# Optimization experiments

Hardware: AMD Instinct MI355X
Metric: run time of the kernel (lower is better)

The kernel has to match this reference:

```python
import jax, jax.numpy as jnp
import numpy as np

N_NODES = 50000
N_EDGES = 800000
F_IN = 16
HEADS = 4
CONV_DIMS = [(16, 16), (16, 32), (32, 32), (32, 32), (32, 32), (32, 64)]
LIN_DIMS = [(128, 256), (256, 64), (64, 16), (16, 1)]


def setup_inputs() -> dict:
    key = jax.random.key(0)
    ks = iter(jax.random.split(key, 64))
    inp = {}
    inp["x"] = jax.random.normal(next(ks), (N_NODES, F_IN), dtype=jnp.float32)
    inp["edge_index"] = jax.random.randint(next(ks), (2, N_EDGES), 0, N_NODES, dtype=jnp.int32)
    for i, (ci, co) in enumerate(CONV_DIMS, 1):
        inp[f"W{i}"] = jax.random.normal(next(ks), (ci, HEADS * co), dtype=jnp.float32) * (1.0 / np.sqrt(ci))
        inp[f"U{i}"] = jax.random.normal(next(ks), (ci, HEADS), dtype=jnp.float32) * (1.0 / np.sqrt(ci))
        inp[f"c{i}"] = jnp.zeros((HEADS,), jnp.float32)
        inp[f"b{i}"] = jnp.zeros((co,), jnp.float32)
    for i, d in zip((1, 2, 3), (32, 32, 64)):
        inp[f"g{i}"] = jnp.ones((d,), jnp.float32)
        inp[f"be{i}"] = jnp.zeros((d,), jnp.float32)
    for name, (ci, co) in zip(("1", "2", "3", "o"), LIN_DIMS):
        inp[f"lw{name}"] = jax.random.normal(next(ks), (ci, co), dtype=jnp.float32) * (1.0 / np.sqrt(ci))
        inp[f"lb{name}"] = jnp.zeros((co,), jnp.float32)
    return inp


def _feast(x, src, dst, W, U, c, b):
    # FeaStConv (PyG): q = softmax_h(U^T (x_j - x_i) + c); out_i = mean_j sum_h q_h * (W_h x_j) + b
    n = x.shape[0]
    out_ch = W.shape[1] // HEADS
    q = jax.nn.softmax((x[src] - x[dst]) @ U + c, axis=-1)            # [E, H]
    xw = (x @ W).reshape(n, HEADS, out_ch)                            # [N, H, O]
    msg = jnp.einsum('eho,eh->eo', xw[src], q)                        # [E, O]
    s = jax.ops.segment_sum(msg, dst, num_segments=n)
    cnt = jax.ops.segment_sum(jnp.ones((src.shape[0], 1), msg.dtype), dst, num_segments=n)
    return s / jnp.maximum(cnt, 1.0) + b


def _bn(x, g, b, eps=1e-5):
    # training-mode BatchNorm over the node dimension
    m = x.mean(0)
    v = x.var(0)
    return (x - m) * jax.lax.rsqrt(v + eps) * g + b


def _forward(x, edge_index, convs, bns, lins):
    # FeaStConv adds self-loops by default
    loops = jnp.arange(x.shape[0], dtype=edge_index.dtype)
    src = jnp.concatenate([edge_index[0], loops])
    dst = jnp.concatenate([edge_index[1], loops])
    h = jax.nn.relu(_feast(x, src, dst, *convs[0]))
    x1 = _bn(jax.nn.relu(_feast(h, src, dst, *convs[1])), *bns[0])
    x2 = jax.nn.relu(_feast(x1, src, dst, *convs[2]))
    x2 = _bn(jax.nn.relu(_feast(x2, src, dst, *convs[3])), *bns[1])
    x3 = jax.nn.relu(_feast(x2, src, dst, *convs[4]))
    x3 = _bn(jax.nn.relu(_feast(x3, src, dst, *convs[5])), *bns[2])
    z = jax.nn.relu(jnp.concatenate([x1, x2, x3], axis=1))            # [N, 128]
    (lw1, lb1), (lw2, lb2), (lw3, lb3), (lwo, lbo) = lins
    z = jax.nn.relu(z @ lw1 + lb1)
    z = jax.nn.relu(z @ lw2 + lb2)
    z = jax.nn.relu(z @ lw3 + lb3)
    return jax.nn.sigmoid(z @ lwo + lbo)                              # [N, 1]


def reference(x, edge_index, W1, U1, c1, b1, W2, U2, c2, b2, W3, U3, c3, b3, W4, U4, c4, b4, W5, U5, c5, b5, W6, U6, c6, b6, g1, be1, g2, be2, g3, be3, lw1, lb1, lw2, lb2, lw3, lb3, lwo, lbo):
    convs = [(W1, U1, c1, b1), (W2, U2, c2, b2), (W3, U3, c3, b3), (W4, U4, c4, b4), (W5, U5, c5, b5), (W6, U6, c6, b6)]
    bns = [(g1, be1), (g2, be2), (g3, be3)]
    lins = [(lw1, lb1), (lw2, lb2), (lw3, lb3), (lwo, lbo)]
    return _forward(x, edge_index, convs, bns, lins)
```

## Files before the change

### kernel.cpp

```cpp
#include <hip/hip_runtime.h>

constexpr int NN = 50000;
constexpr int NE = 800000;
constexpr int SNB = (NN + 255) / 256;

typedef _Float16 h8 __attribute__((ext_vector_type(8)));
typedef _Float16 h4v __attribute__((ext_vector_type(4)));
typedef float f32x4 __attribute__((ext_vector_type(4)));

__global__ void hist_kernel(const int* __restrict__ dst, int* __restrict__ deg) {
    int e = blockIdx.x * blockDim.x + threadIdx.x;
    if (e < NE) atomicAdd(&deg[dst[e]], 1);
}

__global__ __launch_bounds__(256) void scan_bsum_kernel(const int* __restrict__ deg,
                                                        int* __restrict__ bsum) {
    int i = blockIdx.x * 256 + threadIdx.x;
    int v = (i < NN) ? deg[i] : 0;
#pragma unroll
    for (int off = 32; off > 0; off >>= 1) v += __shfl_xor(v, off);
    __shared__ int ws[4];
    if ((threadIdx.x & 63) == 0) ws[threadIdx.x >> 6] = v;
    __syncthreads();
    if (threadIdx.x == 0) bsum[blockIdx.x] = ws[0] + ws[1] + ws[2] + ws[3];
}

__global__ __launch_bounds__(256) void scan_tops_kernel(const int* __restrict__ bsum,
                                                        int* __restrict__ bpre) {
    int tid = threadIdx.x;
    int v = (tid < SNB) ? bsum[tid] : 0;
    int lane = tid & 63, wid = tid >> 6;
    int x = v;
#pragma unroll
    for (int off = 1; off < 64; off <<= 1) {
        int y = __shfl_up(x, off, 64);
        if (lane >= off) x += y;
    }
    __shared__ int wsum[4];
    if (lane == 63) wsum[wid] = x;
    __syncthreads();
    int wpre = 0;
    for (int w = 0; w < wid; w++) wpre += wsum[w];
    if (tid < SNB) bpre[tid] = wpre + x - v;
    if (tid == 0) bpre[SNB] = wsum[0] + wsum[1] + wsum[2] + wsum[3];
}

__global__ __launch_bounds__(256) void scan_final_kernel(const int* __restrict__ deg,
                                                         const int* __restrict__ bpre,
                                                         int* __restrict__ row_ptr,
                                                         int* __restrict__ fillc) {
    int i = blockIdx.x * 256 + threadIdx.x;
    int v = (i < NN) ? deg[i] : 0;
    int lane = threadIdx.x & 63, wid = threadIdx.x >> 6;
    int x = v;
#pragma unroll
    for (int off = 1; off < 64; off <<= 1) {
        int y = __shfl_up(x, off, 64);
        if (lane >= off) x += y;
    }
    __shared__ int wsum[4];
    if (lane == 63) wsum[wid] = x;
    __syncthreads();
    int wpre = 0;
    for (int w = 0; w < wid; w++) wpre += wsum[w];
    int ex = bpre[blockIdx.x] + wpre + x - v;
    if (i < NN) { row_ptr[i] = ex; fillc[i] = ex; }
    if (i == 0) row_ptr[NN] = bpre[SNB];
}

__global__ void fill_kernel(const int* __restrict__ src, const int* __restrict__ dst,
                            int* __restrict__ fillc, int* __restrict__ col) {
    int e = blockIdx.x * blockDim.x + threadIdx.x;
    if (e < NE) {
        int d = dst[e];
        int k = atomicAdd(&fillc[d], 1);
        col[k] = src[e];
    }
}

template <int CI>
__global__ __launch_bounds__(256) void prep_kernel(const float* __restrict__ x,
                                                   const float* __restrict__ U,
                                                   _Float16* __restrict__ xh,
                                                   float* __restrict__ t) {
    __shared__ float Us[CI * 4];
    for (int i = threadIdx.x; i < CI * 4; i += 256) Us[i] = U[i];
    __syncthreads();
    int n = blockIdx.x * 256 + threadIdx.x;
    if (n >= NN) return;
    float xr[CI];
    const float4* xv = reinterpret_cast<const float4*>(x + (size_t)n * CI);
#pragma unroll
    for (int q = 0; q < CI / 4; q++) {
        float4 v = xv[q];
        xr[4 * q + 0] = v.x; xr[4 * q + 1] = v.y; xr[4 * q + 2] = v.z; xr[4 * q + 3] = v.w;
    }
    h8* xo = reinterpret_cast<h8*>(xh + (size_t)n * CI);
#pragma unroll
    for (int q = 0; q < CI / 8; q++) {
        h8 hv;
#pragma unroll
        for (int u = 0; u < 8; u++) hv[u] = (_Float16)xr[8 * q + u];
        xo[q] = hv;
    }
    float a0 = 0.f, a1 = 0.f, a2 = 0.f, a3 = 0.f;
#pragma unroll
    for (int k = 0; k < CI; k++) {
        float xk = xr[k];
        a0 = fmaf(xk, Us[k * 4 + 0], a0); a1 = fmaf(xk, Us[k * 4 + 1], a1);
        a2 = fmaf(xk, Us[k * 4 + 2], a2); a3 = fmaf(xk, Us[k * 4 + 3], a3);
    }
    reinterpret_cast<float4*>(t)[n] = make_float4(a0, a1, a2, a3);
}

__global__ __launch_bounds__(256) void edgeq_kernel(const int* __restrict__ col,
                                                    const int* __restrict__ row_ptr,
                                                    const float* __restrict__ t,
                                                    const float* __restrict__ cvec,
                                                    h4v* __restrict__ qbuf) {
    int n = blockIdx.x * 16 + (threadIdx.x >> 4);
    if (n >= NN) return;
    int l16 = threadIdx.x & 15;
    float4 cv = *reinterpret_cast<const float4*>(cvec);
    float4 td = reinterpret_cast<const float4*>(t)[n];
    float b0 = cv.x - td.x, b1 = cv.y - td.y, b2 = cv.z - td.z, b3 = cv.w - td.w;
    int beg = row_ptr[n], end = row_ptr[n + 1];
    for (int e = beg + l16; e < end; e += 16) {
        int s = col[e];
        float4 ts = reinterpret_cast<const float4*>(t)[s];
        float d0 = ts.x + b0, d1 = ts.y + b1, d2 = ts.z + b2, d3 = ts.w + b3;
        float mm = fmaxf(fmaxf(d0, d1), fmaxf(d2, d3));
        float q0 = __expf(d0 - mm), q1 = __expf(d1 - mm);
        float q2 = __expf(d2 - mm), q3 = __expf(d3 - mm);
        float is = 1.f / (q0 + q1 + q2 + q3);
        h4v q;
        q[0] = (_Float16)(q0 * is); q[1] = (_Float16)(q1 * is);
        q[2] = (_Float16)(q2 * is); q[3] = (_Float16)(q3 * is);
        qbuf[e] = q;
    }
}

template <int CI>
__global__ __launch_bounds__(256) void aggC_kernel(const _Float16* __restrict__ xh,
                                                   const h4v* __restrict__ qbuf,
                                                   const float* __restrict__ cvec,
                                                   const int* __restrict__ row_ptr,
                                                   const int* __restrict__ col,
                                                   _Float16* __restrict__ y) {
    constexpr int SLOTS = 128 / CI;
    __shared__ float part[2][CI * 4];
    int tid = threadIdx.x;
    int half = tid >> 7;
    int lt = tid & 127;
    int n = blockIdx.x * 2 + half;
    int ch = lt & (CI - 1);
    int slot = lt / CI;
    float4 cv = *reinterpret_cast<const float4*>(cvec);
    float a0 = 0.f, a1 = 0.f, a2 = 0.f, a3 = 0.f;
    if (slot == 0) {
        float m = fmaxf(fmaxf(cv.x, cv.y), fmaxf(cv.z, cv.w));
        float s0 = __expf(cv.x - m), s1 = __expf(cv.y - m),
              s2 = __expf(cv.z - m), s3 = __expf(cv.w - m);
        float sinv = 1.f / (s0 + s1 + s2 + s3);
        float xself = (float)xh[(size_t)n * CI + ch];
        a0 = s0 * sinv * xself; a1 = s1 * sinv * xself;
        a2 = s2 * sinv * xself; a3 = s3 * sinv * xself;
    }
    int beg = row_ptr[n], end = row_ptr[n + 1];
#pragma unroll 4
    for (int e = beg + slot; e < end; e += SLOTS) {
        int s = col[e];
        h4v q = qbuf[e];
        float xv = (float)xh[(size_t)s * CI + ch];
        a0 = fmaf((float)q[0], xv, a0); a1 = fmaf((float)q[1], xv, a1);
        a2 = fmaf((float)q[2], xv, a2); a3 = fmaf((float)q[3], xv, a3);
    }
#pragma unroll
    for (int off = 32; off >= CI; off >>= 1) {
        a0 += __shfl_xor(a0, off); a1 += __shfl_xor(a1, off);
        a2 += __shfl_xor(a2, off); a3 += __shfl_xor(a3, off);
    }
    if (lt >= 64 && lt < 64 + CI) {
        part[half][ch * 4 + 0] = a0; part[half][ch * 4 + 1] = a1;
        part[half][ch * 4 + 2] = a2; part[half][ch * 4 + 3] = a3;
    }
    __syncthreads();
    if (lt < CI) {
        a0 += part[half][ch * 4 + 0]; a1 += part[half][ch * 4 + 1];
        a2 += part[half][ch * 4 + 2]; a3 += part[half][ch * 4 + 3];
        float sc = 1.f / (float)(end - beg + 1);
        _Float16* yo = y + (size_t)n * 4 * CI + ch;
        yo[0]      = (_Float16)(a0 * sc);
        yo[CI]     = (_Float16)(a1 * sc);
        yo[2 * CI] = (_Float16)(a2 * sc);
        yo[3 * CI] = (_Float16)(a3 * sc);
    }
}

template <int K, int CO, int COB, bool STACKED, bool OUT16, bool TPREP>
__global__ __launch_bounds__(256) void mfma_dense_kernel(const _Float16* __restrict__ A,
                                                         const float* __restrict__ W,
                                                         const float* __restrict__ bias,
                                                         const float* __restrict__ U,
                                                         void* __restrict__ outp,
                                                         float* __restrict__ tout) {
    constexpr int KS = K / 16;
    constexpr int OT = COB / 16;
    constexpr int CIc = K / 4;
    __shared__ _Float16 Bf[OT * KS * 64 * 4];
    __shared__ float bS[COB];
    __shared__ float Us[TPREP ? CO * 4 : 4];
    int o0 = blockIdx.y * COB;
    for (int idx = threadIdx.x; idx < OT * KS * 64; idx += 256) {
        int lane = idx & 63;
        int ks = (idx >> 6) % KS;
        int ot = idx / (64 * KS);
        int o = o0 + ot * 16 + (lane & 15);
        int kb = ks * 16 + (lane >> 4) * 4;
        h4v v;
#pragma unroll
        for (int j = 0; j < 4; j++) {
            int k = kb + j;
            float wv;
            if constexpr (STACKED) wv = W[(k % CIc) * (4 * CO) + (k / CIc) * CO + o];
            else                   wv = W[k * CO + o];
            v[j] = (_Float16)wv;
        }
        *reinterpret_cast<h4v*>(&Bf[idx * 4]) = v;
    }
    for (int i = threadIdx.x; i < COB; i += 256) bS[i] = bias[o0 + i];
    if constexpr (TPREP) {
        for (int i = threadIdx.x; i < CO * 4; i += 256) Us[i] = U[i];
    }
    __syncthreads();
    int wid = threadIdx.x >> 6, lane = threadIdx.x & 63;
    int row_in = lane & 15;
    int kgrp = lane >> 4;
    for (int mt = blockIdx.x * 4 + wid; mt < NN / 16; mt += gridDim.x * 4) {
        int m0 = mt * 16;
        f32x4 acc[OT];
#pragma unroll
        for (int t = 0; t < OT; t++) acc[t] = {0.f, 0.f, 0.f, 0.f};
        const _Float16* Ab = A + (size_t)(m0 + row_in) * K + kgrp * 4;
#pragma unroll
        for (int ks = 0; ks < KS; ks++) {
            h4v af = *reinterpret_cast<const h4v*>(Ab + ks * 16);
#pragma unroll
            for (int t = 0; t < OT; t++) {
                h4v bf = *reinterpret_cast<const h4v*>(&Bf[((t * KS + ks) * 64 + lane) * 4]);
                acc[t] = __builtin_amdgcn_mfma_f32_16x16x16f16(af, bf, acc[t], 0, 0, 0);
            }
        }
        int orow0 = m0 + kgrp * 4;
#pragma unroll
        for (int t = 0; t < OT; t++) {
            int colo = o0 + t * 16 + row_in;
            float b = bS[t * 16 + row_in];
#pragma unroll
            for (int i = 0; i < 4; i++) {
                float v = fmaxf(acc[t][i] + b, 0.f);
                acc[t][i] = v;
                if constexpr (OUT16)
                    ((_Float16*)outp)[(size_t)(orow0 + i) * CO + colo] = (_Float16)v;
                else
                    ((float*)outp)[(size_t)(orow0 + i) * CO + colo] = v;
            }
        }
        if constexpr (TPREP) {
            float p[4][4];
#pragma unroll
            for (int i = 0; i < 4; i++)
#pragma unroll
                for (int h = 0; h < 4; h++) p[i][h] = 0.f;
#pragma unroll
            for (int tt = 0; tt < OT; tt++) {
                const float* ur = &Us[(tt * 16 + row_in) * 4];
#pragma unroll
                for (int i = 0; i < 4; i++) {
                    float v = acc[tt][i];
#pragma unroll
                    for (int h = 0; h < 4; h++) p[i][h] = fmaf(v, ur[h], p[i][h]);
                }
            }
#pragma unroll
            for (int mask = 1; mask < 16; mask <<= 1) {
#pragma unroll
                for (int i = 0; i < 4; i++)
#pragma unroll
                    for (int h = 0; h < 4; h++) p[i][h] += __shfl_xor(p[i][h], mask);
            }
            tout[(size_t)(orow0 + (row_in >> 2)) * 4 + (row_in & 3)] = p[row_in >> 2][row_in & 3];
        }
    }
}

template <int C>
__global__ __launch_bounds__(256) void bn_reduce_kernel(const float* __restrict__ a,
                                                        float* __restrict__ stats) {
    constexpr int R = 256 / C;
    int cidx = threadIdx.x % C;
    int r = threadIdx.x / C;
    float s = 0.f, s2 = 0.f;
    for (int n = blockIdx.x * R + r; n < NN; n += gridDim.x * R) {
        float v = a[(size_t)n * C + cidx];
        s += v; s2 = fmaf(v, v, s2);
    }
    __shared__ float ls[256], ls2[256];
    ls[threadIdx.x] = s; ls2[threadIdx.x] = s2;
    __syncthreads();
    for (int off = 128; off >= C; off >>= 1) {
        if (threadIdx.x < off) {
            ls[threadIdx.x] += ls[threadIdx.x + off];
            ls2[threadIdx.x] += ls2[threadIdx.x + off];
        }
        __syncthreads();
    }
    if (threadIdx.x < C) {
        atomicAdd(&stats[cidx], ls[threadIdx.x]);
        atomicAdd(&stats[C + cidx], ls2[threadIdx.x]);
    }
}

template <int C>
__global__ __launch_bounds__(256) void bn_norm_prep_kernel(const float* __restrict__ a,
                                                           const float* __restrict__ stats,
                                                           const float* __restrict__ g,
                                                           const float* __restrict__ be,
                                                           const float* __restrict__ U,
                                                           _Float16* __restrict__ xh,
                                                           float* __restrict__ t,
                                                           _Float16* __restrict__ zh,
                                                           int zoff) {
    __shared__ float mS[C], sS[C], beS[C], Us[C * 4];
    if (threadIdx.x < C) {
        int c = threadIdx.x;
        float mean = stats[c] * (1.f / NN);
        float var = stats[C + c] * (1.f / NN) - mean * mean;
        mS[c] = mean;
        sS[c] = rsqrtf(fmaxf(var, 0.f) + 1e-5f) * g[c];
        beS[c] = be[c];
    }
    for (int i = threadIdx.x; i < C * 4; i += 256) Us[i] = U[i];
    __syncthreads();
    int n = blockIdx.x * 256 + threadIdx.x;
    if (n >= NN) return;
    const float4* ap = reinterpret_cast<const float4*>(a + (size_t)n * C);
    h8* xo = reinterpret_cast<h8*>(xh + (size_t)n * C);
    h8* zo = reinterpret_cast<h8*>(zh + (size_t)n * 128 + zoff);
    float t0 = 0.f, t1 = 0.f, t2 = 0.f, t3 = 0.f;
#pragma unroll
    for (int q8 = 0; q8 < C / 8; q8++) {
        h8 hv, zv;
#pragma unroll
        for (int q4 = 0; q4 < 2; q4++) {
            int c4 = q8 * 2 + q4;
            float4 v = ap[c4];
            float r0 = (v.x - mS[c4 * 4 + 0]) * sS[c4 * 4 + 0] + beS[c4 * 4 + 0];
            float r1 = (v.y - mS[c4 * 4 + 1]) * sS[c4 * 4 + 1] + beS[c4 * 4 + 1];
            float r2 = (v.z - mS[c4 * 4 + 2]) * sS[c4 * 4 + 2] + beS[c4 * 4 + 2];
            float r3 = (v.w - mS[c4 * 4 + 3]) * sS[c4 * 4 + 3] + beS[c4 * 4 + 3];
            hv[q4 * 4 + 0] = (_Float16)r0; hv[q4 * 4 + 1] = (_Float16)r1;
            hv[q4 * 4 + 2] = (_Float16)r2; hv[q4 * 4 + 3] = (_Float16)r3;
            zv[q4 * 4 + 0] = (_Float16)fmaxf(r0, 0.f); zv[q4 * 4 + 1] = (_Float16)fmaxf(r1, 0.f);
            zv[q4 * 4 + 2] = (_Float16)fmaxf(r2, 0.f); zv[q4 * 4 + 3] = (_Float16)fmaxf(r3, 0.f);
            const float* us;
            us = &Us[(c4 * 4 + 0) * 4];
            t0 = fmaf(r0, us[0], t0); t1 = fmaf(r0, us[1], t1); t2 = fmaf(r0, us[2], t2); t3 = fmaf(r0, us[3], t3);
            us = &Us[(c4 * 4 + 1) * 4];
            t0 = fmaf(r1, us[0], t0); t1 = fmaf(r1, us[1], t1); t2 = fmaf(r1, us[2], t2); t3 = fmaf(r1, us[3], t3);
            us = &Us[(c4 * 4 + 2) * 4];
            t0 = fmaf(r2, us[0], t0); t1 = fmaf(r2, us[1], t1); t2 = fmaf(r2, us[2], t2); t3 = fmaf(r2, us[3], t3);
            us = &Us[(c4 * 4 + 3) * 4];
            t0 = fmaf(r3, us[0], t0); t1 = fmaf(r3, us[1], t1); t2 = fmaf(r3, us[2], t2); t3 = fmaf(r3, us[3], t3);
        }
        xo[q8] = hv;
        zo[q8] = zv;
    }
    reinterpret_cast<float4*>(t)[n] = make_float4(t0, t1, t2, t3);
}

template <int C>
__global__ __launch_bounds__(256) void bn_norm_z_kernel(const float* __restrict__ a,
                                                        const float* __restrict__ stats,
                                                        const float* __restrict__ g,
                                                        const float* __restrict__ be,
                                                        _Float16* __restrict__ zh,
                                                        int zoff) {
    __shared__ float mS[C], sS[C], beS[C];
    if (threadIdx.x < C) {
        int c = threadIdx.x;
        float mean = stats[c] * (1.f / NN);
        float var = stats[C + c] * (1.f / NN) - mean * mean;
        mS[c] = mean;
        sS[c] = rsqrtf(fmaxf(var, 0.f) + 1e-5f) * g[c];
        beS[c] = be[c];
    }
    __syncthreads();
    int n = blockIdx.x * 256 + threadIdx.x;
    if (n >= NN) return;
    const float4* ap = reinterpret_cast<const float4*>(a + (size_t)n * C);
    h8* zo = reinterpret_cast<h8*>(zh + (size_t)n * 128 + zoff);
#pragma unroll
    for (int q8 = 0; q8 < C / 8; q8++) {
        h8 zv;
#pragma unroll
        for (int q4 = 0; q4 < 2; q4++) {
            int c4 = q8 * 2 + q4;
            float4 v = ap[c4];
            zv[q4 * 4 + 0] = (_Float16)fmaxf((v.x - mS[c4 * 4 + 0]) * sS[c4 * 4 + 0] + beS[c4 * 4 + 0], 0.f);
            zv[q4 * 4 + 1] = (_Float16)fmaxf((v.y - mS[c4 * 4 + 1]) * sS[c4 * 4 + 1] + beS[c4 * 4 + 1], 0.f);
            zv[q4 * 4 + 2] = (_Float16)fmaxf((v.z - mS[c4 * 4 + 2]) * sS[c4 * 4 + 2] + beS[c4 * 4 + 2], 0.f);
            zv[q4 * 4 + 3] = (_Float16)fmaxf((v.w - mS[c4 * 4 + 3]) * sS[c4 * 4 + 3] + beS[c4 * 4 + 3], 0.f);
        }
        zo[q8] = zv;
    }
}

__global__ __launch_bounds__(256) void lin3o_kernel(const _Float16* __restrict__ z2,
                                                    const float* __restrict__ lw3,
                                                    const float* __restrict__ lb3,
                                                    const float* __restrict__ lwo,
                                                    const float* __restrict__ lbo,
                                                    float* __restrict__ out) {
    __shared__ float W3s[64 * 16];
    __shared__ float Wos[16];
    __shared__ float b3s[16];
    for (int i = threadIdx.x; i < 64 * 16; i += 256) W3s[i] = lw3[i];
    if (threadIdx.x < 16) { Wos[threadIdx.x] = lwo[threadIdx.x]; b3s[threadIdx.x] = lb3[threadIdx.x]; }
    __syncthreads();
    int n = blockIdx.x * 256 + threadIdx.x;
    if (n >= NN) return;
    float acc[16];
#pragma unroll
    for (int u = 0; u < 16; u++) acc[u] = b3s[u];
    const h8* zp = reinterpret_cast<const h8*>(z2 + (size_t)n * 64);
#pragma unroll
    for (int k8 = 0; k8 < 8; k8++) {
        h8 v = zp[k8];
#pragma unroll
        for (int u = 0; u < 8; u++) {
            float vf = (float)v[u];
            const float* w = &W3s[(k8 * 8 + u) * 16];
#pragma unroll
            for (int o = 0; o < 16; o++) acc[o] = fmaf(vf, w[o], acc[o]);
        }
    }
    float s = lbo[0];
#pragma unroll
    for (int u = 0; u < 16; u++) s = fmaf(fmaxf(acc[u], 0.f), Wos[u], s);
    out[n] = 1.f / (1.f + __expf(-s));
}

extern "C" void kernel_launch(void* const* d_in, const int* in_sizes, int n_in,
                              void* d_out, int out_size, void* d_ws, size_t ws_size,
                              hipStream_t stream) {
    const float* x = (const float*)d_in[0];
    const int* ei = (const int*)d_in[1];
    const int* esrc = ei;
    const int* edst = ei + NE;
    const float* W[6]; const float* U[6]; const float* C[6]; const float* B[6];
    for (int i = 0; i < 6; i++) {
        W[i] = (const float*)d_in[2 + 4 * i];
        U[i] = (const float*)d_in[3 + 4 * i];
        C[i] = (const float*)d_in[4 + 4 * i];
        B[i] = (const float*)d_in[5 + 4 * i];
    }
    const float* g1 = (const float*)d_in[26]; const float* be1 = (const float*)d_in[27];
    const float* g2 = (const float*)d_in[28]; const float* be2 = (const float*)d_in[29];
    const float* g3 = (const float*)d_in[30]; const float* be3 = (const float*)d_in[31];
    const float* lw1 = (const float*)d_in[32]; const float* lb1 = (const float*)d_in[33];
    const float* lw2 = (const float*)d_in[34]; const float* lb2 = (const float*)d_in[35];
    const float* lw3 = (const float*)d_in[36]; const float* lb3 = (const float*)d_in[37];
    const float* lwo = (const float*)d_in[38]; const float* lbo = (const float*)d_in[39];

    char* w = (char*)d_ws;
    size_t o = 0;
    auto take = [&](size_t bytes) -> char* {
        char* p = w + o;
        o = (o + bytes + 255) & ~(size_t)255;
        return p;
    };
    int* deg = (int*)take((size_t)NN * 4);
    float* stats = (float*)take(3 * 256 * 4);
    size_t zero_bytes = o;
    int* fillc = (int*)take((size_t)NN * 4);
    int* row_ptr = (int*)take((size_t)(NN + 1) * 4);
    int* bsum = (int*)take((size_t)(SNB + 1) * 4);
    int* bpre = (int*)take((size_t)(SNB + 1) * 4);
    int* colA = (int*)take((size_t)NE * 4);
    h4v* qbuf = (h4v*)take((size_t)NE * 8);
    float* t = (float*)take((size_t)NN * 4 * 4);
    _Float16* xh = (_Float16*)take((size_t)NN * 32 * 2);
    char* A = take((size_t)NN * 256 * 2);
    _Float16* y = (_Float16*)A;
    _Float16* z1h = (_Float16*)A;
    _Float16* zh = (_Float16*)take((size_t)NN * 128 * 2);
    float* tmp = (float*)take((size_t)NN * 64 * 4);
    _Float16* z2h = (_Float16*)tmp;
    float* st0 = stats, *st1 = stats + 256, *st2 = stats + 512;

    hipMemsetAsync(d_ws, 0, zero_bytes, stream);

    const int EB = (NE + 255) / 256;
    const int NB = (NN + 255) / 256;
    const int QB = (NN + 15) / 16;
    const int GB = 250;

    hist_kernel<<<EB, 256, 0, stream>>>(edst, deg);
    scan_bsum_kernel<<<SNB, 256, 0, stream>>>(deg, bsum);
    scan_tops_kernel<<<1, 256, 0, stream>>>(bsum, bpre);
    scan_final_kernel<<<SNB, 256, 0, stream>>>(deg, bpre, row_ptr, fillc);
    fill_kernel<<<EB, 256, 0, stream>>>(esrc, edst, fillc, colA);

    prep_kernel<16><<<NB, 256, 0, stream>>>(x, U[0], xh, t);
    edgeq_kernel<<<QB, 256, 0, stream>>>(colA, row_ptr, t, C[0], qbuf);
    aggC_kernel<16><<<NN / 2, 256, 0, stream>>>(xh, qbuf, C[0], row_ptr, colA, y);
    mfma_dense_kernel<64, 16, 16, true, true, true><<<dim3(GB, 1), 256, 0, stream>>>(y, W[0], B[0], U[1], xh, t);
    edgeq_kernel<<<QB, 256, 0, stream>>>(colA, row_ptr, t, C[1], qbuf);
    aggC_kernel<16><<<NN / 2, 256, 0, stream>>>(xh, qbuf, C[1], row_ptr, colA, y);
    mfma_dense_kernel<64, 32, 32, true, false, false><<<dim3(GB, 1), 256, 0, stream>>>(y, W[1], B[1], nullptr, tmp, nullptr);
    bn_reduce_kernel<32><<<256, 256, 0, stream>>>(tmp, st0);
    bn_norm_prep_kernel<32><<<NB, 256, 0, stream>>>(tmp, st0, g1, be1, U[2], xh, t, zh, 0);
    edgeq_kernel<<<QB, 256, 0, stream>>>(colA, row_ptr, t, C[2], qbuf);
    aggC_kernel<32><<<NN / 2, 256, 0, stream>>>(xh, qbuf, C[2], row_ptr, colA, y);
    mfma_dense_kernel<128, 32, 32, true, true, true><<<dim3(GB, 1), 256, 0, stream>>>(y, W[2], B[2], U[3], xh, t);
    edgeq_kernel<<<QB, 256, 0, stream>>>(colA, row_ptr, t, C[3], qbuf);
    aggC_kernel<32><<<NN / 2, 256, 0, stream>>>(xh, qbuf, C[3], row_ptr, colA, y);
    mfma_dense_kernel<128, 32, 32, true, false, false><<<dim3(GB, 1), 256, 0, stream>>>(y, W[3], B[3], nullptr, tmp, nullptr);
    bn_reduce_kernel<32><<<256, 256, 0, stream>>>(tmp, st1);
    bn_norm_prep_kernel<32><<<NB, 256, 0, stream>>>(tmp, st1, g2, be2, U[4], xh, t, zh, 32);
    edgeq_kernel<<<QB, 256, 0, stream>>>(colA, row_ptr, t, C[4], qbuf);
    aggC_kernel<32><<<NN / 2, 256, 0, stream>>>(xh, qbuf, C[4], row_ptr, colA, y);
    mfma_dense_kernel<128, 32, 32, true, true, true><<<dim3(GB, 1), 256, 0, stream>>>(y, W[4], B[4], U[5], xh, t);
    edgeq_kernel<<<QB, 256, 0, stream>>>(colA, row_ptr, t, C[5], qbuf);
    aggC_kernel<32><<<NN / 2, 256, 0, stream>>>(xh, qbuf, C[5], row_ptr, colA, y);
    mfma_dense_kernel<128, 64, 64, true, false, false><<<dim3(GB, 1), 256, 0, stream>>>(y, W[5], B[5], nullptr, tmp, nullptr);
    bn_reduce_kernel<64><<<256, 256, 0, stream>>>(tmp, st2);
    bn_norm_z_kernel<64><<<NB, 256, 0, stream>>>(tmp, st2, g3, be3, zh, 64);

    mfma_dense_kernel<128, 256, 64, false, true, false><<<dim3(GB, 4), 256, 0, stream>>>(zh, lw1, lb1, nullptr, z1h, nullptr);
    mfma_dense_kernel<256, 64, 64, false, true, false><<<dim3(GB, 1), 256, 0, stream>>>(z1h, lw2, lb2, nullptr, z2h, nullptr);
    lin3o_kernel<<<NB, 256, 0, stream>>>(z2h, lw3, lb3, lwo, lbo, (float*)d_out);
}
```

Baseline: 695.1 us.

## Fuse edge softmax computation into aggregation kernel via shared-memory staging

```diff
diff --git a/kernel.cpp b/kernel.cpp
--- a/kernel.cpp
+++ b/kernel.cpp
@@ -113,49 +113,24 @@
     reinterpret_cast<float4*>(t)[n] = make_float4(a0, a1, a2, a3);
 }
 
-__global__ __launch_bounds__(256) void edgeq_kernel(const int* __restrict__ col,
-                                                    const int* __restrict__ row_ptr,
-                                                    const float* __restrict__ t,
-                                                    const float* __restrict__ cvec,
-                                                    h4v* __restrict__ qbuf) {
-    int n = blockIdx.x * 16 + (threadIdx.x >> 4);
-    if (n >= NN) return;
-    int l16 = threadIdx.x & 15;
-    float4 cv = *reinterpret_cast<const float4*>(cvec);
-    float4 td = reinterpret_cast<const float4*>(t)[n];
-    float b0 = cv.x - td.x, b1 = cv.y - td.y, b2 = cv.z - td.z, b3 = cv.w - td.w;
-    int beg = row_ptr[n], end = row_ptr[n + 1];
-    for (int e = beg + l16; e < end; e += 16) {
-        int s = col[e];
-        float4 ts = reinterpret_cast<const float4*>(t)[s];
-        float d0 = ts.x + b0, d1 = ts.y + b1, d2 = ts.z + b2, d3 = ts.w + b3;
-        float mm = fmaxf(fmaxf(d0, d1), fmaxf(d2, d3));
-        float q0 = __expf(d0 - mm), q1 = __expf(d1 - mm);
-        float q2 = __expf(d2 - mm), q3 = __expf(d3 - mm);
-        float is = 1.f / (q0 + q1 + q2 + q3);
-        h4v q;
-        q[0] = (_Float16)(q0 * is); q[1] = (_Float16)(q1 * is);
-        q[2] = (_Float16)(q2 * is); q[3] = (_Float16)(q3 * is);
-        qbuf[e] = q;
-    }
-}
-
 template <int CI>
-__global__ __launch_bounds__(256) void aggC_kernel(const _Float16* __restrict__ xh,
-                                                   const h4v* __restrict__ qbuf,
+__global__ __launch_bounds__(128) void aggD_kernel(const _Float16* __restrict__ xh,
+                                                   const float* __restrict__ t,
                                                    const float* __restrict__ cvec,
                                                    const int* __restrict__ row_ptr,
                                                    const int* __restrict__ col,
                                                    _Float16* __restrict__ y) {
-    constexpr int SLOTS = 128 / CI;
-    __shared__ float part[2][CI * 4];
+    constexpr int NSLOT = 128 / CI;
+    __shared__ int ss[128];
+    __shared__ float4 qs[128];
+    __shared__ float part[CI * 4];
     int tid = threadIdx.x;
-    int half = tid >> 7;
-    int lt = tid & 127;
-    int n = blockIdx.x * 2 + half;
-    int ch = lt & (CI - 1);
-    int slot = lt / CI;
+    int n = blockIdx.x;
+    int ch = tid & (CI - 1);
+    int slot = tid / CI;
     float4 cv = *reinterpret_cast<const float4*>(cvec);
+    float4 td = reinterpret_cast<const float4*>(t)[n];
+    float b0 = cv.x - td.x, b1 = cv.y - td.y, b2 = cv.z - td.z, b3 = cv.w - td.w;
     float a0 = 0.f, a1 = 0.f, a2 = 0.f, a3 = 0.f;
     if (slot == 0) {
         float m = fmaxf(fmaxf(cv.x, cv.y), fmaxf(cv.z, cv.w));
@@ -167,27 +142,44 @@
         a2 = s2 * sinv * xself; a3 = s3 * sinv * xself;
     }
     int beg = row_ptr[n], end = row_ptr[n + 1];
+    for (int base = beg; base < end; base += 128) {
+        int m = end - base;
+        if (m > 128) m = 128;
+        if (tid < m) {
+            int s = col[base + tid];
+            float4 ts = reinterpret_cast<const float4*>(t)[s];
+            float d0 = ts.x + b0, d1 = ts.y + b1, d2 = ts.z + b2, d3 = ts.w + b3;
+            float mm = fmaxf(fmaxf(d0, d1), fmaxf(d2, d3));
+            float q0 = __expf(d0 - mm), q1 = __expf(d1 - mm);
+            float q2 = __expf(d2 - mm), q3 = __expf(d3 - mm);
+            float is = 1.f / (q0 + q1 + q2 + q3);
+            ss[tid] = s;
+            qs[tid] = make_float4(q0 * is, q1 * is, q2 * is, q3 * is);
+        }
+        __syncthreads();
 #pragma unroll 4
-    for (int e = beg + slot; e < end; e += SLOTS) {
-        int s = col[e];
-        h4v q = qbuf[e];
-        float xv = (float)xh[(size_t)s * CI + ch];
-        a0 = fmaf((float)q[0], xv, a0); a1 = fmaf((float)q[1], xv, a1);
-        a2 = fmaf((float)q[2], xv, a2); a3 = fmaf((float)q[3], xv, a3);
+        for (int j = slot; j < m; j += NSLOT) {
+            int s = ss[j];
+            float4 q = qs[j];
+            float xv = (float)xh[(size_t)s * CI + ch];
+            a0 = fmaf(q.x, xv, a0); a1 = fmaf(q.y, xv, a1);
+            a2 = fmaf(q.z, xv, a2); a3 = fmaf(q.w, xv, a3);
+        }
+        __syncthreads();
     }
 #pragma unroll
     for (int off = 32; off >= CI; off >>= 1) {
         a0 += __shfl_xor(a0, off); a1 += __shfl_xor(a1, off);
         a2 += __shfl_xor(a2, off); a3 += __shfl_xor(a3, off);
     }
-    if (lt >= 64 && lt < 64 + CI) {
-        part[half][ch * 4 + 0] = a0; part[half][ch * 4 + 1] = a1;
-        part[half][ch * 4 + 2] = a2; part[half][ch * 4 + 3] = a3;
-    }
-    __syncthreads();
-    if (lt < CI) {
-        a0 += part[half][ch * 4 + 0]; a1 += part[half][ch * 4 + 1];
-        a2 += part[half][ch * 4 + 2]; a3 += part[half][ch * 4 + 3];
+    if (tid >= 64 && tid < 64 + CI) {
+        part[ch * 4 + 0] = a0; part[ch * 4 + 1] = a1;
+        part[ch * 4 + 2] = a2; part[ch * 4 + 3] = a3;
+    }
+    __syncthreads();
+    if (tid < CI) {
+        a0 += part[ch * 4 + 0]; a1 += part[ch * 4 + 1];
+        a2 += part[ch * 4 + 2]; a3 += part[ch * 4 + 3];
         float sc = 1.f / (float)(end - beg + 1);
         _Float16* yo = y + (size_t)n * 4 * CI + ch;
         yo[0]      = (_Float16)(a0 * sc);
@@ -488,7 +480,6 @@
     int* bsum = (int*)take((size_t)(SNB + 1) * 4);
     int* bpre = (int*)take((size_t)(SNB + 1) * 4);
     int* colA = (int*)take((size_t)NE * 4);
-    h4v* qbuf = (h4v*)take((size_t)NE * 8);
     float* t = (float*)take((size_t)NN * 4 * 4);
     _Float16* xh = (_Float16*)take((size_t)NN * 32 * 2);
     char* A = take((size_t)NN * 256 * 2);
@@ -503,7 +494,6 @@
 
     const int EB = (NE + 255) / 256;
     const int NB = (NN + 255) / 256;
-    const int QB = (NN + 15) / 16;
     const int GB = 250;
 
     hist_kernel<<<EB, 256, 0, stream>>>(edst, deg);
@@ -513,27 +503,21 @@
     fill_kernel<<<EB, 256, 0, stream>>>(esrc, edst, fillc, colA);
 
     prep_kernel<16><<<NB, 256, 0, stream>>>(x, U[0], xh, t);
-    edgeq_kernel<<<QB, 256, 0, stream>>>(colA, row_ptr, t, C[0], qbuf);
-    aggC_kernel<16><<<NN / 2, 256, 0, stream>>>(xh, qbuf, C[0], row_ptr, colA, y);
+    aggD_kernel<16><<<NN, 128, 0, stream>>>(xh, t, C[0], row_ptr, colA, y);
     mfma_dense_kernel<64, 16, 16, true, true, true><<<dim3(GB, 1), 256, 0, stream>>>(y, W[0], B[0], U[1], xh, t);
-    edgeq_kernel<<<QB, 256, 0, stream>>>(colA, row_ptr, t, C[1], qbuf);
-    aggC_kernel<16><<<NN / 2, 256, 0, stream>>>(xh, qbuf, C[1], row_ptr, colA, y);
+    aggD_kernel<16><<<NN, 128, 0, stream>>>(xh, t, C[1], row_ptr, colA, y);
     mfma_dense_kernel<64, 32, 32, true, false, false><<<dim3(GB, 1), 256, 0, stream>>>(y, W[1], B[1], nullptr, tmp, nullptr);
     bn_reduce_kernel<32><<<256, 256, 0, stream>>>(tmp, st0);
     bn_norm_prep_kernel<32><<<NB, 256, 0, stream>>>(tmp, st0, g1, be1, U[2], xh, t, zh, 0);
-    edgeq_kernel<<<QB, 256, 0, stream>>>(colA, row_ptr, t, C[2], qbuf);
-    aggC_kernel<32><<<NN / 2, 256, 0, stream>>>(xh, qbuf, C[2], row_ptr, colA, y);
+    aggD_kernel<32><<<NN, 128, 0, stream>>>(xh, t, C[2], row_ptr, colA, y);
     mfma_dense_kernel<128, 32, 32, true, true, true><<<dim3(GB, 1), 256, 0, stream>>>(y, W[2], B[2], U[3], xh, t);
-    edgeq_kernel<<<QB, 256, 0, stream>>>(colA, row_ptr, t, C[3], qbuf);
-    aggC_kernel<32><<<NN / 2, 256, 0, stream>>>(xh, qbuf, C[3], row_ptr, colA, y);
+    aggD_kernel<32><<<NN, 128, 0, stream>>>(xh, t, C[3], row_ptr, colA, y);
     mfma_dense_kernel<128, 32, 32, true, false, false><<<dim3(GB, 1), 256, 0, stream>>>(y, W[3], B[3], nullptr, tmp, nullptr);
     bn_reduce_kernel<32><<<256, 256, 0, stream>>>(tmp, st1);
     bn_norm_prep_kernel<32><<<NB, 256, 0, stream>>>(tmp, st1, g2, be2, U[4], xh, t, zh, 32);
-    edgeq_kernel<<<QB, 256, 0, stream>>>(colA, row_ptr, t, C[4], qbuf);
-    aggC_kernel<32><<<NN / 2, 256, 0, stream>>>(xh, qbuf, C[4], row_ptr, colA, y);
+    aggD_kernel<32><<<NN, 128, 0, stream>>>(xh, t, C[4], row_ptr, colA, y);
     mfma_dense_kernel<128, 32, 32, true, true, true><<<dim3(GB, 1), 256, 0, stream>>>(y, W[4], B[4], U[5], xh, t);
-    edgeq_kernel<<<QB, 256, 0, stream>>>(colA, row_ptr, t, C[5], qbuf);
-    aggC_kernel<32><<<NN / 2, 256, 0, stream>>>(xh, qbuf, C[5], row_ptr, colA, y);
+    aggD_kernel<32><<<NN, 128, 0, stream>>>(xh, t, C[5], row_ptr, colA, y);
     mfma_dense_kernel<128, 64, 64, true, false, false><<<dim3(GB, 1), 256, 0, stream>>>(y, W[5], B[5], nullptr, tmp, nullptr);
     bn_reduce_kernel<64><<<256, 256, 0, stream>>>(tmp, st2);
     bn_norm_z_kernel<64><<<NB, 256, 0, stream>>>(tmp, st2, g3, be3, zh, 64);
```

Measured after the change: 625.7 us. 10.0% less time.
